# Kernel tuning notes

Measured on AMD Instinct MI355X. Metric: run time of the kernel, lower is better.

The kernel has to match this reference:

```python
import jax, jax.numpy as jnp
import numpy as np


def setup_inputs() -> dict:
    key = jax.random.key(0)
    B, H, W = 16, 1024, 1024
    x = jax.random.uniform(key, (B, H, W), dtype=jnp.float32)
    return {"x": x, "bit_depth": 1}


def reference(x, bit_depth):
    # --- reduce_color_depth: quantize via truncating int cast (torch .int()) ---
    scale = 255.0 / (2 ** bit_depth - 1)
    xq = jnp.trunc(x * scale) / scale

    # --- spatial_smoothing: 3x3 median filter with reflect padding ---
    B, H, W = xq.shape
    xp = jnp.pad(xq, ((0, 0), (1, 1), (1, 1)), mode="reflect")  # [B, H+2, W+2]
    # stack the 9 shifted views -> [B, H, W, 9] (same as unfold+view)
    patches = jnp.stack(
        [xp[:, i:i + H, j:j + W] for i in range(3) for j in range(3)], axis=-1
    )
    # odd window (9) -> median is the middle order statistic, matching torch.median
    return jnp.median(patches, axis=-1)
```

## Files before the change

kernel.cpp:

```cpp
#include <hip/hip_runtime.h>
#include <math.h>


constexpr int H = 1024;
constexpr int W = 1024;
constexpr int TY = 8;

__device__ __forceinline__ float min3f(float a, float b, float c) { return fminf(a, fminf(b, c)); }
__device__ __forceinline__ float max3f(float a, float b, float c) { return fmaxf(a, fmaxf(b, c)); }
__device__ __forceinline__ float med3f(float a, float b, float c) { return __builtin_amdgcn_fmed3f(a, b, c); }

__global__ __launch_bounds__(256) void fsq_kernel(const float* __restrict__ x,
                                                  const int* __restrict__ bdp,
                                                  float* __restrict__ out) {
    const int t    = threadIdx.x;
    const int lane = t & 63;
    const int y0   = blockIdx.x * TY;
    const int b    = blockIdx.y;

    const float q     = (float)((1 << bdp[0]) - 1);
    const float scale = 255.0f / q;
    const float rinv  = q / 255.0f;

    const size_t base = (size_t)b * H * W;
    const float* __restrict__ xb = x + base;
    float* __restrict__ ob       = out + base;

    const int c0 = 4 * t;
    const int cEdge = (lane == 0) ? ((c0 == 0) ? 1 : c0 - 1)
                                  : ((c0 + 4 < W) ? c0 + 4 : W - 2);
    const bool isEdge = (lane == 0) | (lane == 63);

    float r0[6], r1[6], r2[6];

    auto loadrow = [&](int gy, float* vv) {
        gy = (gy < 0) ? 1 : ((gy >= H) ? 2 * H - 2 - gy : gy);
        const float* row = xb + (size_t)gy * W;
        const float4 m = *(const float4*)(row + c0);

        float e = 0.0f;
        if (isEdge) e = row[cEdge];

        const float q1 = truncf(m.x * scale) * rinv;
        const float q2 = truncf(m.y * scale) * rinv;
        const float q3 = truncf(m.z * scale) * rinv;
        const float q4 = truncf(m.w * scale) * rinv;
        const float qe = truncf(e   * scale) * rinv;

        float l = __shfl_up(q4, 1, 64);
        float r = __shfl_down(q1, 1, 64);
        if (lane == 0)  l = qe;
        if (lane == 63) r = qe;

        vv[0] = l; vv[1] = q1; vv[2] = q2; vv[3] = q3; vv[4] = q4; vv[5] = r;
    };

    loadrow(y0 - 1, r0);
    loadrow(y0,     r1);

    #pragma unroll
    for (int i = 0; i < TY; ++i) {
        loadrow(y0 + 1 + i, r2);

        float lo[6], mi[6], hi[6];
        #pragma unroll
        for (int c = 0; c < 6; ++c) {
            lo[c] = min3f(r0[c], r1[c], r2[c]);
            mi[c] = med3f(r0[c], r1[c], r2[c]);
            hi[c] = max3f(r0[c], r1[c], r2[c]);
        }

        float4 o;
        o.x = med3f(max3f(lo[0], lo[1], lo[2]), med3f(mi[0], mi[1], mi[2]), min3f(hi[0], hi[1], hi[2]));
        o.y = med3f(max3f(lo[1], lo[2], lo[3]), med3f(mi[1], mi[2], mi[3]), min3f(hi[1], hi[2], hi[3]));
        o.z = med3f(max3f(lo[2], lo[3], lo[4]), med3f(mi[2], mi[3], mi[4]), min3f(hi[2], hi[3], hi[4]));
        o.w = med3f(max3f(lo[3], lo[4], lo[5]), med3f(mi[3], mi[4], mi[5]), min3f(hi[3], hi[4], hi[5]));
        *(float4*)(ob + (size_t)(y0 + i) * W + c0) = o;

        #pragma unroll
        for (int c = 0; c < 6; ++c) { r0[c] = r1[c]; r1[c] = r2[c]; }
    }
}

extern "C" void kernel_launch(void* const* d_in, const int* in_sizes, int n_in,
                              void* d_out, int out_size, void* d_ws, size_t ws_size,
                              hipStream_t stream) {
    const float* x  = (const float*)d_in[0];
    const int*   bd = (const int*)d_in[1];
    float*       out = (float*)d_out;

    const int B = in_sizes[0] / (H * W);
    dim3 grid(H / TY, B);
    fsq_kernel<<<grid, 256, 0, stream>>>(x, bd, out);
}
```

Before: 116.8 us.

## Hoist all row loads up front and quantize after median instead of before

Issues all TY+2 row loads (float4 plus edge value) at kernel start so the memory requests are in flight together instead of interleaved with compute. It also moves the truncating quantization from every loaded element to the four output values, relying on quantization being monotonic so it commutes with the median. This cuts the trunc/multiply work roughly threefold and raises memory-level parallelism, at the cost of more registers held live.

```diff
diff --git a/kernel.cpp b/kernel.cpp
--- a/kernel.cpp
+++ b/kernel.cpp
@@ -5,6 +5,7 @@
 constexpr int H = 1024;
 constexpr int W = 1024;
 constexpr int TY = 8;
+constexpr int NR = TY + 2;
 
 __device__ __forceinline__ float min3f(float a, float b, float c) { return fminf(a, fminf(b, c)); }
 __device__ __forceinline__ float max3f(float a, float b, float c) { return fmaxf(a, fmaxf(b, c)); }
@@ -31,36 +32,34 @@
                                   : ((c0 + 4 < W) ? c0 + 4 : W - 2);
     const bool isEdge = (lane == 0) | (lane == 63);
 
+    float4 m[NR];
+    float  e[NR];
+    #pragma unroll
+    for (int r = 0; r < NR; ++r) {
+        int gy = y0 - 1 + r;
+        gy = (gy < 0) ? 1 : ((gy >= H) ? 2 * H - 2 - gy : gy);
+        const float* row = xb + (size_t)gy * W;
+        m[r] = *(const float4*)(row + c0);
+        e[r] = 0.0f;
+        if (isEdge) e[r] = row[cEdge];
+    }
+
     float r0[6], r1[6], r2[6];
 
-    auto loadrow = [&](int gy, float* vv) {
-        gy = (gy < 0) ? 1 : ((gy >= H) ? 2 * H - 2 - gy : gy);
-        const float* row = xb + (size_t)gy * W;
-        const float4 m = *(const float4*)(row + c0);
-
-        float e = 0.0f;
-        if (isEdge) e = row[cEdge];
-
-        const float q1 = truncf(m.x * scale) * rinv;
-        const float q2 = truncf(m.y * scale) * rinv;
-        const float q3 = truncf(m.z * scale) * rinv;
-        const float q4 = truncf(m.w * scale) * rinv;
-        const float qe = truncf(e   * scale) * rinv;
-
-        float l = __shfl_up(q4, 1, 64);
-        float r = __shfl_down(q1, 1, 64);
-        if (lane == 0)  l = qe;
-        if (lane == 63) r = qe;
-
-        vv[0] = l; vv[1] = q1; vv[2] = q2; vv[3] = q3; vv[4] = q4; vv[5] = r;
+    auto mkrow = [&](int r, float* vv) {
+        float l  = __shfl_up(m[r].w, 1, 64);
+        float rr = __shfl_down(m[r].x, 1, 64);
+        if (lane == 0)  l  = e[r];
+        if (lane == 63) rr = e[r];
+        vv[0] = l; vv[1] = m[r].x; vv[2] = m[r].y; vv[3] = m[r].z; vv[4] = m[r].w; vv[5] = rr;
     };
 
-    loadrow(y0 - 1, r0);
-    loadrow(y0,     r1);
+    mkrow(0, r0);
+    mkrow(1, r1);
 
     #pragma unroll
     for (int i = 0; i < TY; ++i) {
-        loadrow(y0 + 1 + i, r2);
+        mkrow(2 + i, r2);
 
         float lo[6], mi[6], hi[6];
         #pragma unroll
@@ -75,6 +74,11 @@
         o.y = med3f(max3f(lo[1], lo[2], lo[3]), med3f(mi[1], mi[2], mi[3]), min3f(hi[1], hi[2], hi[3]));
         o.z = med3f(max3f(lo[2], lo[3], lo[4]), med3f(mi[2], mi[3], mi[4]), min3f(hi[2], hi[3], hi[4]));
         o.w = med3f(max3f(lo[3], lo[4], lo[5]), med3f(mi[3], mi[4], mi[5]), min3f(hi[3], hi[4], hi[5]));
+
+        o.x = truncf(o.x * scale) * rinv;
+        o.y = truncf(o.y * scale) * rinv;
+        o.z = truncf(o.z * scale) * rinv;
+        o.w = truncf(o.w * scale) * rinv;
         *(float4*)(ob + (size_t)(y0 + i) * W + c0) = o;
 
         #pragma unroll
```

After: 112.2 us. 1.04x faster.
